# Kernel tuning notes

Measured on AMD Instinct MI355X. Metric: run time of the kernel, lower is better.

The kernel has to match this reference:

```python
import jax, jax.numpy as jnp
import numpy as np

# Tensor layout: x is [b, c, d, h, w, p, q, r] = [batch, channels, D, H, W, pd, ph, pw]
LETTERS = 'bcdhwpqr'

def axial_linear(x, W, b, axis, S, C):
    """LinearAlongDims1 over dims [1, axis]: jointly mixes channels and one
    spatial/patch axis. Torch flattens in (spatial, channel) order, so the
    (S*C, S*C) weight is reshaped to [S_out, C_out, S_in, C_in]."""
    a = LETTERS[axis]
    W4 = W.reshape(S, C, S, C)
    out_sub = LETTERS.replace('c', 'Y').replace(a, 'X')
    y = jnp.einsum(f'{LETTERS},XY{a}c->{out_sub}', x, W4)
    bshape = [1] * 8
    bshape[1] = C
    bshape[axis] = S
    return y + b.reshape(S, C).T.reshape(bshape)


def _make_linear_params(key, n):
    kw, kb = jax.random.split(key)
    bound = 1.0 / np.sqrt(n)
    W = jax.random.uniform(kw, (n, n), jnp.float32, -bound, bound)
    b = jax.random.uniform(kb, (n,), jnp.float32, -bound, bound)
    return W, b


def setup_inputs() -> dict:
    key = jax.random.key(0)
    ks = jax.random.split(key, 7)
    B, C, D, P = 2, 64, 16, 4
    x = jax.random.normal(ks[0], (B, C, D, D, D, P, P, P), jnp.float32)
    w_d, b_d = _make_linear_params(ks[1], C * D)      # image_d: dims [1,2]
    w_h, b_h = _make_linear_params(ks[2], C * D)      # image_h: dims [1,3]
    w_w, b_w = _make_linear_params(ks[3], C * D)      # image_w: dims [1,4]
    w_pd, b_pd = _make_linear_params(ks[4], C * P)    # patch_d: dims [1,5]
    w_ph, b_ph = _make_linear_params(ks[5], C * P)    # patch_h: dims [1,6]
    w_pw, b_pw = _make_linear_params(ks[6], C * P)    # patch_w: dims [1,7]
    return {
        'x': x,
        'w_d': w_d, 'b_d': b_d, 'w_h': w_h, 'b_h': b_h, 'w_w': w_w, 'b_w': b_w,
        'w_pd': w_pd, 'b_pd': b_pd, 'w_ph': w_ph, 'b_ph': b_ph,
        'w_pw': w_pw, 'b_pw': b_pw,
    }


def reference(x, w_d, b_d, w_h, b_h, w_w, b_w,
              w_pd, b_pd, w_ph, b_ph, w_pw, b_pw):
    C = x.shape[1]
    D = x.shape[2]
    P = x.shape[5]
    y = axial_linear(x, w_pd, b_pd, 5, P, C)
    y = y + axial_linear(x, w_ph, b_ph, 6, P, C)
    y = y + axial_linear(x, w_pw, b_pw, 7, P, C)
    y = y + axial_linear(x, w_d, b_d, 2, D, C)
    y = y + axial_linear(x, w_h, b_h, 3, D, C)
    y = y + axial_linear(x, w_w, b_w, 4, D, C)
    # shapes match -> leaky_relu + residual (module returns y; gn(x) is discarded)
    y = x + jax.nn.leaky_relu(y, negative_slope=0.01)
    return y
```

## Files before the change

### kernel.cpp

```cpp
#include <hip/hip_runtime.h>

typedef __attribute__((ext_vector_type(8))) short short8;
typedef __attribute__((ext_vector_type(4))) float floatx4;


__device__ __forceinline__ unsigned short f2bf(float f){
  unsigned int u = __float_as_uint(f);
  u += 0x7FFFu + ((u >> 16) & 1u);
  return (unsigned short)(u >> 16);
}

template<int AX>
__device__ __forceinline__ int tidx(int m, int a, int c){
  if      (AX==0){ int b=m>>14, t=m&16383;                         return (b<<24)|(c<<18)|(a<<14)|t; }
  else if (AX==1){ int b=m>>14, d=(m>>10)&15, t=m&1023;            return (b<<24)|(c<<18)|(d<<14)|(a<<10)|t; }
  else           { int b=m>>14, d=(m>>10)&15, h=(m>>6)&15, t=m&63; return (b<<24)|(c<<18)|(d<<14)|(h<<10)|(a<<6)|t; }
}

template<int AX>
__device__ __forceinline__ int srcbase(int m){
  if      (AX==0) return ((m>>14)<<24) | (((m>>10)&15)<<16) | (((m>>6)&15)<<12) | ((m&63)<<6);
  else if (AX==1) return ((m>>14)<<24) | (((m>>10)&15)<<20) | (((m>>6)&15)<<12) | ((m&63)<<6);
  else            return ((m>>14)<<24) | (((m>>10)&15)<<20) | (((m>>6)&15)<<16) | ((m&63)<<6);
}

#define ASYNC_CP16(g, l) \
  __builtin_amdgcn_global_load_lds( \
      (const __attribute__((address_space(1))) unsigned int*)(g), \
      (__attribute__((address_space(3))) unsigned int*)(l), 16, 0, 0)

__global__ __launch_bounds__(256) void castw_all(
    const float* __restrict__ wa, const float* __restrict__ wb, const float* __restrict__ wc,
    const float* __restrict__ wd_, const float* __restrict__ we, const float* __restrict__ wf,
    const float* __restrict__ bd_, const float* __restrict__ bh_, const float* __restrict__ bw_,
    const float* __restrict__ bpd_, const float* __restrict__ bph_, const float* __restrict__ bpw_,
    unsigned short* oa, unsigned short* ob, unsigned short* oc,
    unsigned short* od, unsigned short* oe, unsigned short* of_,
    float* __restrict__ Bimg, float* __restrict__ Bpat){
  int blk = blockIdx.x;
  if (blk < 6528){
    const float* src; unsigned short* dst; int idx;
    if (blk < 6144){ int wsel = blk >> 11, loc = blk & 2047;
      src = wsel==0?wa:(wsel==1?wb:wc); dst = wsel==0?oa:(wsel==1?ob:oc);
      idx = loc*256 + threadIdx.x; }
    else { int b2 = blk - 6144, wsel = b2 >> 7, loc = b2 & 127;
      src = wsel==0?wd_:(wsel==1?we:wf); dst = wsel==0?od:(wsel==1?oe:of_);
      idx = loc*256 + threadIdx.x; }
    float2 v = ((const float2*)src)[idx];
    ((unsigned int*)dst)[idx] = (unsigned int)f2bf(v.x) | ((unsigned int)f2bf(v.y) << 16);
  } else if (blk < 7552){
    int idx = (blk - 6528)*256 + threadIdx.x;
    int c = idx & 63, wv = (idx>>6)&15, hv = (idx>>10)&15, dv = idx>>14;
    Bimg[idx] = bd_[dv*64+c] + bh_[hv*64+c] + bw_[wv*64+c];
  } else {
    int idx = (blk - 7552)*256 + threadIdx.x;
    int c = idx & 63, tt = idx>>6;
    int p = tt>>4, q = (tt>>2)&3, r = tt&3;
    Bpat[idx] = bpd_[p*64+c] + bph_[q*64+c] + bpw_[r*64+c];
  }
}

__global__ __launch_bounds__(256) void transpose_cx(const float* __restrict__ x,
                                                    unsigned short* __restrict__ xt){
  __shared__ float T[64][65];
  int b  = blockIdx.x >> 12;
  int s0 = (blockIdx.x & 4095) * 64;
  int t = threadIdx.x;
  int cr = t >> 4, sq = t & 15;
  #pragma unroll
  for (int it = 0; it < 4; it++){
    int c = it*16 + cr;
    float4 v = *(const float4*)(x + (b<<24) + (c<<18) + s0 + sq*4);
    T[c][sq*4+0]=v.x; T[c][sq*4+1]=v.y; T[c][sq*4+2]=v.z; T[c][sq*4+3]=v.w;
  }
  __syncthreads();
  int sw = t >> 2, cq = t & 3;
  unsigned int pk[8];
  #pragma unroll
  for (int i=0;i<8;i++){
    float f0 = T[cq*16 + 2*i    ][sw];
    float f1 = T[cq*16 + 2*i + 1][sw];
    pk[i] = (unsigned int)f2bf(f0) | ((unsigned int)f2bf(f1) << 16);
  }
  uint4* dst = (uint4*)(xt + (b<<24) + ((s0 + sw)<<6) + cq*16);
  dst[0] = make_uint4(pk[0],pk[1],pk[2],pk[3]);
  dst[1] = make_uint4(pk[4],pk[5],pk[6],pk[7]);
}

template<int AXI, bool FIRST>
__device__ __forceinline__ void patch_axis(const unsigned short* Xs,
                                           const unsigned short* __restrict__ W,
                                           float* AccL, int w, int l16, int q8){
  floatx4 acc[4][2];
  #pragma unroll
  for (int nt=0;nt<4;nt++)
    #pragma unroll
    for (int mt=0;mt<2;mt++) acc[nt][mt] = (floatx4){0.f,0.f,0.f,0.f};

  #pragma unroll 2
  for (int kit = 0; kit < 8; kit++){
    int a = kit >> 1;
    short8 bf[2], af[4];
    int u = (AXI==0) ? (a*16 + l16)
          : (AXI==1) ? ((l16>>2)*16 + a*4 + (l16&3))
                     : ((l16>>2)*16 + (l16&3)*4 + a);
    int jg = ((kit & 1) << 2) + q8;
    #pragma unroll
    for (int mt = 0; mt < 2; mt++){
      int r = mt*64 + u;
      int j = jg ^ ((r ^ (r >> 3)) & 7);
      bf[mt] = *(const short8*)(Xs + r*64 + j*8);
    }
    #pragma unroll
    for (int nt = 0; nt < 4; nt++){
      int n = w*64 + nt*16 + l16;
      af[nt] = *(const short8*)(W + n*256 + kit*32 + q8*8);
    }
    #pragma unroll
    for (int nt=0; nt<4; nt++)
      #pragma unroll
      for (int mt=0; mt<2; mt++)
        acc[nt][mt] = __builtin_amdgcn_mfma_f32_16x16x32_bf16(af[nt], bf[mt], acc[nt][mt], 0,0,0);
  }

  int uo = (AXI==0) ? (w*16 + l16)
         : (AXI==1) ? ((l16>>2)*16 + w*4 + (l16&3))
                    : ((l16>>2)*16 + (l16&3)*4 + w);
  #pragma unroll
  for (int nt=0; nt<4; nt++)
    #pragma unroll
    for (int mt=0; mt<2; mt++){
      float* p = AccL + (mt*64 + uo)*65 + nt*16 + q8*4;
      #pragma unroll
      for (int rg=0; rg<4; rg++){
        if (FIRST) p[rg]  = acc[nt][mt][rg];
        else       p[rg] += acc[nt][mt][rg];
      }
    }
}

__global__ __launch_bounds__(256) void patch_fused(const unsigned short* __restrict__ xt,
    const unsigned short* __restrict__ Wp_, const unsigned short* __restrict__ Wq_,
    const unsigned short* __restrict__ Wr_, float* __restrict__ out){
  __shared__ float AccL[2*64*65];
  __shared__ unsigned short Xs[8192];
  int pp = blockIdx.x;
  int b = pp >> 11, dpair = pp & 2047;
  const unsigned short* xp = xt + (b<<24) + dpair*8192;
  int t = threadIdx.x, w = t>>6, lane = t&63, q8 = lane>>4, l16 = lane&15;

  #pragma unroll
  for (int i = 0; i < 4; i++){
    int L = i*256 + t;
    int r = L >> 3, jl = L & 7;
    int jg = jl ^ ((r ^ (r >> 3)) & 7);
    ASYNC_CP16(xp + r*64 + jg*8, Xs + i*2048 + w*512);
  }
  __syncthreads();

  patch_axis<0,true >(Xs, Wp_, AccL, w, l16, q8);
  __syncthreads();
  patch_axis<1,false>(Xs, Wq_, AccL, w, l16, q8);
  __syncthreads();
  patch_axis<2,false>(Xs, Wr_, AccL, w, l16, q8);
  __syncthreads();

  int sbase = dpair*128;
  #pragma unroll
  for (int it = 0; it < 32; it++){
    int lin = it*256 + t;
    int c = lin >> 7, rem = lin & 127, pt = rem >> 6, u = rem & 63;
    out[(b<<24) | (c<<18) | (sbase + pt*64 + u)] = AccL[(pt*64+u)*65 + c];
  }
}

#define WAITV8 asm volatile("s_waitcnt vmcnt(8)" ::: "memory")
#define WAITV0 asm volatile("s_waitcnt vmcnt(0)" ::: "memory")

template<int AX, int EPI>
__global__ __launch_bounds__(256) void gemm_img(const unsigned short* __restrict__ xt,
                                                const unsigned short* __restrict__ Wbf,
                                                float* __restrict__ out,
                                                const float* __restrict__ x,
                                                const float* __restrict__ Bimg,
                                                const float* __restrict__ Bpat){
  constexpr int K  = 1024;
  constexpr int SA = (AX==0)?(1<<20):(AX==1)?(1<<16):(1<<12);
  int Bk = blockIdx.x;
  int mt = Bk >> 3, nt = Bk & 7;

  __shared__ unsigned short Xs0[128*64], Ws0[128*64];
  __shared__ unsigned short Xs1[128*64], Ws1[128*64];

  int t = threadIdx.x, lane = t & 63, wid = t >> 6;
  int wn = (wid & 1) << 6, wm = (wid >> 1) << 6;
  int q8 = lane >> 4, l16 = lane & 15;

  floatx4 acc[4][4];
  #pragma unroll
  for (int i=0;i<4;i++)
    #pragma unroll
    for (int j=0;j<4;j++) acc[i][j] = (floatx4){0.f,0.f,0.f,0.f};

  const unsigned short* Wp = Wbf + (size_t)nt*128*K;

  int rr = t >> 3;
  int jg = (t & 7) ^ ((t >> 3) & 7);
  int baseX[4], baseWo[4];
  #pragma unroll
  for (int c=0;c<4;c++){
    int r = c*32 + rr;
    baseX[c]  = srcbase<AX>(mt*128 + r) + jg*8;
    baseWo[c] = r*K + jg*8;
  }

  int xoff[4], woff[4];
  #pragma unroll
  for (int i=0;i<4;i++){
    int rx = wm + i*16 + l16; xoff[i] = rx*64 + ((q8 ^ (rx & 7)) << 3);
    int rw = wn + i*16 + l16; woff[i] = rw*64 + ((q8 ^ (rw & 7)) << 3);
  }

  #define STAGE_T(a, XS, WS) do { \
    _Pragma("unroll") \
    for (int c=0;c<4;c++){ \
      ASYNC_CP16(xt + baseX[c] + (a)*SA, (XS) + c*2048 + wid*512); \
      ASYNC_CP16(Wp + baseWo[c] + (a)*64, (WS) + c*2048 + wid*512); \
    } } while(0)

  #define COMPUTE_T(XS, WS) do { \
    _Pragma("unroll") \
    for (int kk=0; kk<2; kk++){ \
      short8 wf[4], xf[4]; \
      _Pragma("unroll") \
      for (int i=0;i<4;i++){ \
        wf[i] = *(const short8*)&(WS)[woff[i] ^ (kk<<5)]; \
        xf[i] = *(const short8*)&(XS)[xoff[i] ^ (kk<<5)]; \
      } \
      _Pragma("unroll") \
      for (int i=0;i<4;i++) \
        _Pragma("unroll") \
        for (int j=0;j<4;j++) \
          acc[i][j] = __builtin_amdgcn_mfma_f32_16x16x32_bf16(wf[i], xf[j], acc[i][j], 0,0,0); \
    } } while(0)

  STAGE_T(0, Xs0, Ws0);
  WAITV0;
  __builtin_amdgcn_s_barrier();
  STAGE_T(1, Xs1, Ws1);

  for (int a2 = 0; a2 < 8; a2++){
    COMPUTE_T(Xs0, Ws0);
    __builtin_amdgcn_s_barrier();
    if (a2 < 7){ STAGE_T(2*a2+2, Xs0, Ws0); WAITV8; }
    else       { WAITV0; }
    __builtin_amdgcn_s_barrier();
    COMPUTE_T(Xs1, Ws1);
    if (a2 < 7){
      __builtin_amdgcn_s_barrier();
      STAGE_T(2*a2+3, Xs1, Ws1);
      WAITV8;
      __builtin_amdgcn_s_barrier();
    }
  }
  #undef STAGE_T
  #undef COMPUTE_T

  #pragma unroll
  for (int i=0;i<4;i++){
    #pragma unroll
    for (int j=0;j<4;j++){
      int mg = mt*128 + wm + j*16 + l16;
      if (EPI){
        int d = (mg>>10)&15, h = (mg>>6)&15, tt = mg&63;
        int n0 = nt*128 + wn + i*16 + q8*4;
        int a = n0 >> 6, c0 = n0 & 63;
        float4 bi = *(const float4*)(Bimg + (((d*16 + h)*16 + a)*64 + c0));
        float4 bp = *(const float4*)(Bpat + (tt*64 + c0));
        float bs0 = bi.x + bp.x, bs1 = bi.y + bp.y, bs2 = bi.z + bp.z, bs3 = bi.w + bp.w;
        #pragma unroll
        for (int rg=0; rg<4; rg++){
          int ng = n0 + rg;
          int idx = tidx<AX>(mg, ng>>6, ng&63);
          float bsum = (rg==0)?bs0:(rg==1)?bs1:(rg==2)?bs2:bs3;
          float y = out[idx] + acc[i][j][rg] + bsum;
          out[idx] = x[idx] + (y >= 0.f ? y : 0.01f*y);
        }
      } else {
        #pragma unroll
        for (int rg=0; rg<4; rg++){
          int ng = nt*128 + wn + i*16 + q8*4 + rg;
          int idx = tidx<AX>(mg, ng>>6, ng&63);
          out[idx] += acc[i][j][rg];
        }
      }
    }
  }
}

extern "C" void kernel_launch(void* const* d_in, const int* in_sizes, int n_in,
                              void* d_out, int out_size, void* d_ws, size_t ws_size,
                              hipStream_t stream){
  const float* x = (const float*)d_in[0];
  const float* Wsrc[6] = {(const float*)d_in[1], (const float*)d_in[3], (const float*)d_in[5],
                          (const float*)d_in[7], (const float*)d_in[9], (const float*)d_in[11]};
  const float* Bsrc[6] = {(const float*)d_in[2], (const float*)d_in[4], (const float*)d_in[6],
                          (const float*)d_in[8], (const float*)d_in[10], (const float*)d_in[12]};
  float* out = (float*)d_out;
  char* ws = (char*)d_ws;

  const size_t welems[6] = {1024u*1024u, 1024u*1024u, 1024u*1024u,
                            256u*256u, 256u*256u, 256u*256u};
  size_t wOff[6], o = 0;
  for (int i=0;i<6;i++){ wOff[i] = o; o += welems[i]*2; }
  size_t xtOff = (o + 255) & ~(size_t)255;
  size_t bimgOff = xtOff + ((size_t)1u<<25)*2;
  size_t bpatOff = bimgOff + (size_t)16*16*16*64*4;
  unsigned short* xt = (unsigned short*)(ws + xtOff);
  float* Bimg = (float*)(ws + bimgOff);
  float* Bpat = (float*)(ws + bpatOff);
  unsigned short* Wbf[6];
  for (int i=0;i<6;i++) Wbf[i] = (unsigned short*)(ws + wOff[i]);

  castw_all<<<7616,256,0,stream>>>(Wsrc[0],Wsrc[1],Wsrc[2],Wsrc[3],Wsrc[4],Wsrc[5],
                                   Bsrc[0],Bsrc[1],Bsrc[2],Bsrc[3],Bsrc[4],Bsrc[5],
                                   Wbf[0],Wbf[1],Wbf[2],Wbf[3],Wbf[4],Wbf[5],
                                   Bimg, Bpat);
  transpose_cx<<<8192,256,0,stream>>>(x, xt);

  patch_fused<<<4096,256,0,stream>>>(xt, Wbf[3], Wbf[4], Wbf[5], out);

  gemm_img<0,0><<<2048,256,0,stream>>>(xt, Wbf[0], out, nullptr, nullptr, nullptr);
  gemm_img<1,0><<<2048,256,0,stream>>>(xt, Wbf[1], out, nullptr, nullptr, nullptr);
  gemm_img<2,1><<<2048,256,0,stream>>>(xt, Wbf[2], out, x, Bimg, Bpat);
}
```

Measured before the change: 848.5 us.

## Enlarge image GEMM tiles to 256x256 with 512-thread blocks and grouped block order

The image-axis GEMMs move from 128x128 tiles with 256 threads to 256x256 tiles with 512 threads. Each wave now computes a 128x64 sub-tile with 32 accumulators, which raises operand reuse from LDS and cuts global re-reads of X and W. Block indices are also remapped so that groups of 8 M tiles share the same N tile, aiming for better L2 locality. The cost is 128KB of LDS per block and many more accumulator registers, which limits occupancy, and there are fewer blocks (512) to fill the GPU.

```diff
diff --git a/kernel.cpp b/kernel.cpp
--- a/kernel.cpp
+++ b/kernel.cpp
@@ -178,69 +178,73 @@
 #define WAITV0 asm volatile("s_waitcnt vmcnt(0)" ::: "memory")
 
 template<int AX, int EPI>
-__global__ __launch_bounds__(256) void gemm_img(const unsigned short* __restrict__ xt,
-                                                const unsigned short* __restrict__ Wbf,
-                                                float* __restrict__ out,
-                                                const float* __restrict__ x,
-                                                const float* __restrict__ Bimg,
-                                                const float* __restrict__ Bpat){
+__global__ __launch_bounds__(512, 2) void gemm_img(const unsigned short* __restrict__ xt,
+                                                   const unsigned short* __restrict__ Wbf,
+                                                   float* __restrict__ out,
+                                                   const float* __restrict__ x,
+                                                   const float* __restrict__ Bimg,
+                                                   const float* __restrict__ Bpat){
   constexpr int K  = 1024;
   constexpr int SA = (AX==0)?(1<<20):(AX==1)?(1<<16):(1<<12);
-  int Bk = blockIdx.x;
-  int mt = Bk >> 3, nt = Bk & 7;
-
-  __shared__ unsigned short Xs0[128*64], Ws0[128*64];
-  __shared__ unsigned short Xs1[128*64], Ws1[128*64];
+  int bid = blockIdx.x;
+  int mt = (bid >> 5) * 8 + (bid & 7);
+  int nt = (bid >> 3) & 3;
+
+  __shared__ unsigned short Xs0[256*64], Ws0[256*64];
+  __shared__ unsigned short Xs1[256*64], Ws1[256*64];
 
   int t = threadIdx.x, lane = t & 63, wid = t >> 6;
-  int wn = (wid & 1) << 6, wm = (wid >> 1) << 6;
+  int wnb = (wid & 3) << 6;
+  int wmb = (wid >> 2) << 7;
   int q8 = lane >> 4, l16 = lane & 15;
 
-  floatx4 acc[4][4];
+  floatx4 acc[4][8];
   #pragma unroll
   for (int i=0;i<4;i++)
     #pragma unroll
-    for (int j=0;j<4;j++) acc[i][j] = (floatx4){0.f,0.f,0.f,0.f};
-
-  const unsigned short* Wp = Wbf + (size_t)nt*128*K;
+    for (int j=0;j<8;j++) acc[i][j] = (floatx4){0.f,0.f,0.f,0.f};
+
+  const unsigned short* Wp = Wbf + (size_t)nt*256*K;
 
   int rr = t >> 3;
   int jg = (t & 7) ^ ((t >> 3) & 7);
   int baseX[4], baseWo[4];
   #pragma unroll
   for (int c=0;c<4;c++){
-    int r = c*32 + rr;
-    baseX[c]  = srcbase<AX>(mt*128 + r) + jg*8;
+    int r = c*64 + rr;
+    baseX[c]  = srcbase<AX>(mt*256 + r) + jg*8;
     baseWo[c] = r*K + jg*8;
   }
 
-  int xoff[4], woff[4];
+  int xoff[8], woff[4];
+  #pragma unroll
+  for (int j=0;j<8;j++){
+    int rx = wmb + j*16 + l16; xoff[j] = rx*64 + ((q8 ^ (rx & 7)) << 3);
+  }
   #pragma unroll
   for (int i=0;i<4;i++){
-    int rx = wm + i*16 + l16; xoff[i] = rx*64 + ((q8 ^ (rx & 7)) << 3);
-    int rw = wn + i*16 + l16; woff[i] = rw*64 + ((q8 ^ (rw & 7)) << 3);
+    int rw = wnb + i*16 + l16; woff[i] = rw*64 + ((q8 ^ (rw & 7)) << 3);
   }
 
   #define STAGE_T(a, XS, WS) do { \
     _Pragma("unroll") \
     for (int c=0;c<4;c++){ \
-      ASYNC_CP16(xt + baseX[c] + (a)*SA, (XS) + c*2048 + wid*512); \
-      ASYNC_CP16(Wp + baseWo[c] + (a)*64, (WS) + c*2048 + wid*512); \
+      ASYNC_CP16(xt + baseX[c] + (a)*SA, (XS) + c*4096 + wid*512); \
+      ASYNC_CP16(Wp + baseWo[c] + (a)*64, (WS) + c*4096 + wid*512); \
     } } while(0)
 
   #define COMPUTE_T(XS, WS) do { \
     _Pragma("unroll") \
     for (int kk=0; kk<2; kk++){ \
-      short8 wf[4], xf[4]; \
+      short8 wf[4], xf[8]; \
       _Pragma("unroll") \
-      for (int i=0;i<4;i++){ \
-        wf[i] = *(const short8*)&(WS)[woff[i] ^ (kk<<5)]; \
-        xf[i] = *(const short8*)&(XS)[xoff[i] ^ (kk<<5)]; \
-      } \
+      for (int i=0;i<4;i++) wf[i] = *(const short8*)&(WS)[woff[i] ^ (kk<<5)]; \
+      _Pragma("unroll") \
+      for (int j=0;j<8;j++) xf[j] = *(const short8*)&(XS)[xoff[j] ^ (kk<<5)]; \
       _Pragma("unroll") \
       for (int i=0;i<4;i++) \
         _Pragma("unroll") \
-        for (int j=0;j<4;j++) \
+        for (int j=0;j<8;j++) \
           acc[i][j] = __builtin_amdgcn_mfma_f32_16x16x32_bf16(wf[i], xf[j], acc[i][j], 0,0,0); \
     } } while(0)
 
@@ -269,11 +273,11 @@
   #pragma unroll
   for (int i=0;i<4;i++){
     #pragma unroll
-    for (int j=0;j<4;j++){
-      int mg = mt*128 + wm + j*16 + l16;
+    for (int j=0;j<8;j++){
+      int mg = mt*256 + wmb + j*16 + l16;
       if (EPI){
         int d = (mg>>10)&15, h = (mg>>6)&15, tt = mg&63;
-        int n0 = nt*128 + wn + i*16 + q8*4;
+        int n0 = nt*256 + wnb + i*16 + q8*4;
         int a = n0 >> 6, c0 = n0 & 63;
         float4 bi = *(const float4*)(Bimg + (((d*16 + h)*16 + a)*64 + c0));
         float4 bp = *(const float4*)(Bpat + (tt*64 + c0));
@@ -289,7 +293,7 @@
       } else {
         #pragma unroll
         for (int rg=0; rg<4; rg++){
-          int ng = nt*128 + wn + i*16 + q8*4 + rg;
+          int ng = nt*256 + wnb + i*16 + q8*4 + rg;
           int idx = tidx<AX>(mg, ng>>6, ng&63);
           out[idx] += acc[i][j][rg];
         }
@@ -330,7 +334,7 @@
 
   patch_fused<<<4096,256,0,stream>>>(xt, Wbf[3], Wbf[4], Wbf[5], out);
 
-  gemm_img<0,0><<<2048,256,0,stream>>>(xt, Wbf[0], out, nullptr, nullptr, nullptr);
-  gemm_img<1,0><<<2048,256,0,stream>>>(xt, Wbf[1], out, nullptr, nullptr, nullptr);
-  gemm_img<2,1><<<2048,256,0,stream>>>(xt, Wbf[2], out, x, Bimg, Bpat);
-}
+  gemm_img<0,0><<<512,512,0,stream>>>(xt, Wbf[0], out, nullptr, nullptr, nullptr);
+  gemm_img<1,0><<<512,512,0,stream>>>(xt, Wbf[1], out, nullptr, nullptr, nullptr);
+  gemm_img<2,1><<<512,512,0,stream>>>(xt, Wbf[2], out, x, Bimg, Bpat);
+}
```

Measured after the change: 853.2 us. Within noise of the previous version (+0.6%).
